# Kernel optimization log

Measured on AMD Instinct MI355X. Metric: run time of the kernel, lower is better.

The kernel has to match this reference:

```python
import math
import jax
import jax.numpy as jnp
import numpy as np

SEGMENT_SIZE = 2048   # w (init: segment_size)
DILATION_RATE = 4     # r (init: dilation_rate)
D_MODEL = 1024        # init: d_model


def _sparse_indices(n: int, w: int, r: int, head_idx: int) -> np.ndarray:
    """Static SparsifyIndices: per segment of size w, take tokens offset::r.
    Since r divides w, every segment yields exactly m=w//r indices (no -1 pad).
    Returns flat global token indices, shape (S*m,)."""
    S = n // w
    m = w // r
    off = head_idx % r
    seg_start = np.arange(S, dtype=np.int64)[:, None] * w      # (S,1)
    within = off + r * np.arange(m, dtype=np.int64)[None, :]   # (1,m)
    return (seg_start + within).reshape(-1)


def setup_inputs() -> dict:
    key = jax.random.key(0)
    x = jax.random.normal(key, (4, 8192, D_MODEL), dtype=jnp.float32)
    return {"x": x, "head_idx": 1}


def reference(x, head_idx):
    b, n0, d = x.shape
    w, r = SEGMENT_SIZE, DILATION_RATE
    pad = (-n0) % w
    if pad:
        x = jnp.pad(x, ((0, 0), (0, pad), (0, 0)))
    n = n0 + pad
    idx = _sparse_indices(n, w, r, int(head_idx))  # static, (S*m,)
    S, m = n // w, w // r

    # Gather dilated tokens per segment: (b, S, m, d)
    xg = x[:, idx, :].reshape(b, S, m, d)

    # Softmax attention within each sub-segment (q=k=v=xg)
    scores = jnp.einsum('bsid,bsjd->bsij', xg, xg) / math.sqrt(d)  # (b,S,m,m)
    probs = jax.nn.softmax(scores, axis=-1)
    att = jnp.einsum('bsij,bsjd->bsid', probs, xg).reshape(b, S * m, d)

    # MixOutputs: alpha-weighted scatter-add back to full sequence
    denoms = att.sum(-1)                                       # (b, S*m)
    denom_sums = jnp.zeros((b, n), x.dtype).at[:, idx].add(denoms)
    alphas = denoms / denom_sums[:, idx]                       # (b, S*m)
    out = jnp.zeros((b, n, d), x.dtype).at[:, idx, :].add(att * alphas[..., None])
    return out
```

## Files before the change

kernel.cpp:

```cpp
#include <hip/hip_runtime.h>
#include <hip/hip_bf16.h>


typedef __bf16 bf16_t;
typedef __bf16 bf16x8 __attribute__((ext_vector_type(8)));
typedef float floatx4 __attribute__((ext_vector_type(4)));

#define D_MODEL 1024
#define SEG_W   2048
#define RATE    4
#define M_SUB   512
#define NTOK    8192
#define NSEGT   16
#define XG_ELEMS ((long)NSEGT * M_SUB * D_MODEL)
#define S_ELEMS  ((long)NSEGT * M_SUB * M_SUB)

__device__ __forceinline__ void gload16(const bf16_t* g, bf16_t* l) {
    __builtin_amdgcn_global_load_lds(
        (const __attribute__((address_space(1))) void*)g,
        (__attribute__((address_space(3))) void*)l, 16, 0, 0);
}

__global__ __launch_bounds__(256) void zero_kernel(
    const int* __restrict__ hidp, float* __restrict__ out)
{
    const int off = ((hidp[0] % RATE) + RATE) % RATE;
    const int bid = blockIdx.x;
    const int b = bid / 6144, j = bid % 6144;
    const int q = j / 3, r2 = j % 3;
    const int t = 4 * q + r2 + (r2 >= off ? 1 : 0);
    float4 z = {0.f, 0.f, 0.f, 0.f};
    ((float4*)(out + ((long)b * NTOK + t) * D_MODEL))[threadIdx.x] = z;
}

__global__ __launch_bounds__(256) void gather_kernel(
    const float* __restrict__ x, const int* __restrict__ hidp,
    bf16_t* __restrict__ xg, bf16_t* __restrict__ xgT)
{
    const int off = ((hidp[0] % RATE) + RATE) % RATE;
    const int bid = blockIdx.x;
    const int seg = bid >> 7;
    const int rem = bid & 127;
    const int it  = rem >> 4;
    const int dt  = rem & 15;
    const int b   = seg >> 2, s = seg & 3;

    __shared__ ushort tile[64][65];

    const int t  = threadIdx.x;
    const int r  = t >> 2;
    const int cq = (t & 3) << 4;

    union U8 { bf16x8 v; ushort u[8]; };

    {
        const int  i   = it * 64 + r;
        const long tok = (long)s * SEG_W + off + 4L * i;
        const float* src = x + ((long)b * NTOK + tok) * D_MODEL + dt * 64 + cq;
        float4 f0 = ((const float4*)src)[0];
        float4 f1 = ((const float4*)src)[1];
        float4 f2 = ((const float4*)src)[2];
        float4 f3 = ((const float4*)src)[3];
        U8 lo, hi;
        lo.v[0]=(bf16_t)f0.x; lo.v[1]=(bf16_t)f0.y; lo.v[2]=(bf16_t)f0.z; lo.v[3]=(bf16_t)f0.w;
        lo.v[4]=(bf16_t)f1.x; lo.v[5]=(bf16_t)f1.y; lo.v[6]=(bf16_t)f1.z; lo.v[7]=(bf16_t)f1.w;
        hi.v[0]=(bf16_t)f2.x; hi.v[1]=(bf16_t)f2.y; hi.v[2]=(bf16_t)f2.z; hi.v[3]=(bf16_t)f2.w;
        hi.v[4]=(bf16_t)f3.x; hi.v[5]=(bf16_t)f3.y; hi.v[6]=(bf16_t)f3.z; hi.v[7]=(bf16_t)f3.w;
        bf16_t* dstg = xg + ((long)seg * M_SUB + i) * D_MODEL + dt * 64 + cq;
        *(bf16x8*)(dstg)     = lo.v;
        *(bf16x8*)(dstg + 8) = hi.v;
        #pragma unroll
        for (int j = 0; j < 8; ++j) { tile[r][cq + j] = lo.u[j]; tile[r][cq + 8 + j] = hi.u[j]; }
    }
    __syncthreads();
    {
        const int dc = r;
        const int iq = cq;
        U8 o0, o1;
        #pragma unroll
        for (int j = 0; j < 8; ++j) { o0.u[j] = tile[iq + j][dc]; o1.u[j] = tile[iq + 8 + j][dc]; }
        bf16_t* dstT = xgT + ((long)seg * D_MODEL + dt * 64 + dc) * M_SUB + it * 64 + iq;
        *(bf16x8*)(dstT)     = o0.v;
        *(bf16x8*)(dstT + 8) = o1.v;
    }
}

__global__ __launch_bounds__(256) void qk_kernel(
    const bf16_t* __restrict__ xg, bf16_t* __restrict__ S)
{
    const int bid = blockIdx.x;
    const int seg = bid >> 5;
    const int mt  = (bid >> 2) & 7;
    const int nt  = bid & 3;

    const int tid  = threadIdx.x;
    const int w    = tid >> 6;
    const int lane = tid & 63;
    const int l16  = lane & 15;
    const int quad = lane >> 4;
    const int wr   = w >> 1, wc = w & 1;

    __shared__ alignas(16) bf16_t As[64 * 32];
    __shared__ alignas(16) bf16_t Bs[128 * 32];

    const bf16_t* xseg = xg + (long)seg * M_SUB * D_MODEL;
    const bf16_t* ga  = xseg + (long)(mt * 64 + w * 16 + (lane >> 2)) * D_MODEL + (lane & 3) * 8;
    const bf16_t* gb0 = xseg + (long)(nt * 128 + (w * 2 + 0) * 16 + (lane >> 2)) * D_MODEL + (lane & 3) * 8;
    const bf16_t* gb1 = xseg + (long)(nt * 128 + (w * 2 + 1) * 16 + (lane >> 2)) * D_MODEL + (lane & 3) * 8;
    bf16_t* la  = &As[w * 512];
    bf16_t* lb0 = &Bs[(w * 2 + 0) * 512];
    bf16_t* lb1 = &Bs[(w * 2 + 1) * 512];

    floatx4 acc[2][4];
    #pragma unroll
    for (int i = 0; i < 2; ++i)
        #pragma unroll
        for (int j = 0; j < 4; ++j) acc[i][j] = (floatx4){0.f, 0.f, 0.f, 0.f};

    for (int kk = 0; kk < D_MODEL; kk += 32) {
        __syncthreads();
        gload16(ga  + kk, la);
        gload16(gb0 + kk, lb0);
        gload16(gb1 + kk, lb1);
        __syncthreads();

        bf16x8 Af[2], Bf[4];
        #pragma unroll
        for (int m2 = 0; m2 < 2; ++m2)
            Af[m2] = *(const bf16x8*)&As[(wr * 32 + m2 * 16 + l16) * 32 + quad * 8];
        #pragma unroll
        for (int n2 = 0; n2 < 4; ++n2)
            Bf[n2] = *(const bf16x8*)&Bs[(wc * 64 + n2 * 16 + l16) * 32 + quad * 8];
        #pragma unroll
        for (int m2 = 0; m2 < 2; ++m2)
            #pragma unroll
            for (int n2 = 0; n2 < 4; ++n2)
                acc[m2][n2] = __builtin_amdgcn_mfma_f32_16x16x32_bf16(Af[m2], Bf[n2], acc[m2][n2], 0, 0, 0);
    }

    const float scale = 0.03125f;
    bf16_t* Sseg = S + (long)seg * M_SUB * M_SUB;
    #pragma unroll
    for (int m2 = 0; m2 < 2; ++m2) {
        const int qrow = mt * 64 + wr * 32 + m2 * 16 + quad * 4;
        #pragma unroll
        for (int n2 = 0; n2 < 4; ++n2) {
            const int col = nt * 128 + wc * 64 + n2 * 16 + l16;
            #pragma unroll
            for (int rg = 0; rg < 4; ++rg)
                Sseg[(long)(qrow + rg) * M_SUB + col] = (bf16_t)(acc[m2][n2][rg] * scale);
        }
    }
}

__global__ __launch_bounds__(256) void softmax_kernel(bf16_t* __restrict__ S)
{
    const int row  = blockIdx.x * 4 + (threadIdx.x >> 6);
    const int lane = threadIdx.x & 63;
    bf16_t* p = S + (long)row * M_SUB + lane * 8;
    bf16x8 v = *(const bf16x8*)p;
    float f[8];
    #pragma unroll
    for (int j = 0; j < 8; ++j) f[j] = (float)v[j];
    float m = f[0];
    #pragma unroll
    for (int j = 1; j < 8; ++j) m = fmaxf(m, f[j]);
    #pragma unroll
    for (int d = 1; d < 64; d <<= 1) m = fmaxf(m, __shfl_xor(m, d, 64));
    float sum = 0.f;
    #pragma unroll
    for (int j = 0; j < 8; ++j) { f[j] = __expf(f[j] - m); sum += f[j]; }
    #pragma unroll
    for (int d = 1; d < 64; d <<= 1) sum += __shfl_xor(sum, d, 64);
    const float inv = 1.0f / sum;
    #pragma unroll
    for (int j = 0; j < 8; ++j) v[j] = (bf16_t)(f[j] * inv);
    *(bf16x8*)p = v;
}

__global__ __launch_bounds__(256) void pv_kernel(
    const bf16_t* __restrict__ S, const bf16_t* __restrict__ xgT,
    const int* __restrict__ hidp, float* __restrict__ out)
{
    const int off = ((hidp[0] % RATE) + RATE) % RATE;
    const int bid = blockIdx.x;
    const int seg = bid >> 5;
    const int mt  = (bid >> 3) & 3;
    const int nt  = bid & 7;
    const int b   = seg >> 2, s = seg & 3;

    const int tid  = threadIdx.x;
    const int w    = tid >> 6;
    const int lane = tid & 63;
    const int l16  = lane & 15;
    const int quad = lane >> 4;
    const int wr   = w >> 1, wc = w & 1;

    __shared__ alignas(16) bf16_t As[128 * 32];
    __shared__ alignas(16) bf16_t Bs[128 * 32];

    const bf16_t* Aseg = S   + (long)seg * M_SUB * M_SUB + (long)mt * 128 * M_SUB;
    const bf16_t* Bseg = xgT + (long)seg * D_MODEL * M_SUB + (long)nt * 128 * M_SUB;

    const bf16_t* ga0 = Aseg + (long)((w * 2 + 0) * 16 + (lane >> 2)) * M_SUB + (lane & 3) * 8;
    const bf16_t* ga1 = Aseg + (long)((w * 2 + 1) * 16 + (lane >> 2)) * M_SUB + (lane & 3) * 8;
    const bf16_t* gb0 = Bseg + (long)((w * 2 + 0) * 16 + (lane >> 2)) * M_SUB + (lane & 3) * 8;
    const bf16_t* gb1 = Bseg + (long)((w * 2 + 1) * 16 + (lane >> 2)) * M_SUB + (lane & 3) * 8;
    bf16_t* la0 = &As[(w * 2 + 0) * 512];
    bf16_t* la1 = &As[(w * 2 + 1) * 512];
    bf16_t* lb0 = &Bs[(w * 2 + 0) * 512];
    bf16_t* lb1 = &Bs[(w * 2 + 1) * 512];

    floatx4 acc[4][4];
    #pragma unroll
    for (int i = 0; i < 4; ++i)
        #pragma unroll
        for (int j = 0; j < 4; ++j) acc[i][j] = (floatx4){0.f, 0.f, 0.f, 0.f};

    for (int kk = 0; kk < M_SUB; kk += 32) {
        __syncthreads();
        gload16(ga0 + kk, la0);
        gload16(ga1 + kk, la1);
        gload16(gb0 + kk, lb0);
        gload16(gb1 + kk, lb1);
        __syncthreads();

        bf16x8 Af[4], Bf[4];
        #pragma unroll
        for (int m2 = 0; m2 < 4; ++m2)
            Af[m2] = *(const bf16x8*)&As[(wr * 64 + m2 * 16 + l16) * 32 + quad * 8];
        #pragma unroll
        for (int n2 = 0; n2 < 4; ++n2)
            Bf[n2] = *(const bf16x8*)&Bs[(wc * 64 + n2 * 16 + l16) * 32 + quad * 8];
        #pragma unroll
        for (int m2 = 0; m2 < 4; ++m2)
            #pragma unroll
            for (int n2 = 0; n2 < 4; ++n2)
                acc[m2][n2] = __builtin_amdgcn_mfma_f32_16x16x32_bf16(Af[m2], Bf[n2], acc[m2][n2], 0, 0, 0);
    }

    float* obase = out + (long)b * NTOK * D_MODEL;
    #pragma unroll
    for (int m2 = 0; m2 < 4; ++m2) {
        const int qrow0 = mt * 128 + wr * 64 + m2 * 16 + quad * 4;
        #pragma unroll
        for (int rg = 0; rg < 4; ++rg) {
            const long tok = (long)s * SEG_W + off + 4L * (qrow0 + rg);
            float* orow = obase + tok * D_MODEL;
            #pragma unroll
            for (int n2 = 0; n2 < 4; ++n2) {
                const int d = nt * 128 + wc * 64 + n2 * 16 + l16;
                orow[d] = acc[m2][n2][rg];
            }
        }
    }
}

extern "C" void kernel_launch(void* const* d_in, const int* in_sizes, int n_in,
                              void* d_out, int out_size, void* d_ws, size_t ws_size,
                              hipStream_t stream) {
    const float* x   = (const float*)d_in[0];
    const int*   hid = (const int*)d_in[1];
    float*       out = (float*)d_out;
    bf16_t* xg  = (bf16_t*)d_ws;
    bf16_t* xgT = xg + XG_ELEMS;
    bf16_t* S   = xgT + XG_ELEMS;

    zero_kernel<<<dim3(24576), dim3(256), 0, stream>>>(hid, out);
    gather_kernel<<<dim3(2048), dim3(256), 0, stream>>>(x, hid, xg, xgT);
    qk_kernel<<<dim3(512), dim3(256), 0, stream>>>(xg, S);
    softmax_kernel<<<dim3(2048), dim3(256), 0, stream>>>(S);
    pv_kernel<<<dim3(512), dim3(256), 0, stream>>>(S, xgT, hid, out);
}
```

Before: 254.5 us.

## Fuse zero-fill into PV kernel, widen K-tiles to 64 with XOR-swizzled LDS

Removes the separate zero kernel and writes the zeros for non-selected tokens from the PV kernel, each block covering its own 128-row by 128-column tile region, using nontemporal stores. Both GEMM kernels move from K-step 32 to K-step 64 with an XOR-swizzled LDS layout, halving the number of barrier pairs and avoiding bank conflicts on the fragment reads. Output stores also become nontemporal. The cost is more LDS per block, which may lower occupancy, and extra store traffic at the tail of the PV kernel.

```diff
diff --git a/kernel.cpp b/kernel.cpp
--- a/kernel.cpp
+++ b/kernel.cpp
@@ -13,24 +13,11 @@
 #define NTOK    8192
 #define NSEGT   16
 #define XG_ELEMS ((long)NSEGT * M_SUB * D_MODEL)
-#define S_ELEMS  ((long)NSEGT * M_SUB * M_SUB)
 
 __device__ __forceinline__ void gload16(const bf16_t* g, bf16_t* l) {
     __builtin_amdgcn_global_load_lds(
         (const __attribute__((address_space(1))) void*)g,
         (__attribute__((address_space(3))) void*)l, 16, 0, 0);
-}
-
-__global__ __launch_bounds__(256) void zero_kernel(
-    const int* __restrict__ hidp, float* __restrict__ out)
-{
-    const int off = ((hidp[0] % RATE) + RATE) % RATE;
-    const int bid = blockIdx.x;
-    const int b = bid / 6144, j = bid % 6144;
-    const int q = j / 3, r2 = j % 3;
-    const int t = 4 * q + r2 + (r2 >= off ? 1 : 0);
-    float4 z = {0.f, 0.f, 0.f, 0.f};
-    ((float4*)(out + ((long)b * NTOK + t) * D_MODEL))[threadIdx.x] = z;
 }
 
 __global__ __launch_bounds__(256) void gather_kernel(
@@ -99,17 +86,27 @@
     const int l16  = lane & 15;
     const int quad = lane >> 4;
     const int wr   = w >> 1, wc = w & 1;
-
-    __shared__ alignas(16) bf16_t As[64 * 32];
-    __shared__ alignas(16) bf16_t Bs[128 * 32];
+    const int rowin = lane >> 3;
+    const int cswz  = ((lane & 7) ^ rowin) * 8;
+    const int rsw   = l16 & 7;
+
+    __shared__ alignas(16) bf16_t As[64 * 64];
+    __shared__ alignas(16) bf16_t Bs[128 * 64];
 
     const bf16_t* xseg = xg + (long)seg * M_SUB * D_MODEL;
-    const bf16_t* ga  = xseg + (long)(mt * 64 + w * 16 + (lane >> 2)) * D_MODEL + (lane & 3) * 8;
-    const bf16_t* gb0 = xseg + (long)(nt * 128 + (w * 2 + 0) * 16 + (lane >> 2)) * D_MODEL + (lane & 3) * 8;
-    const bf16_t* gb1 = xseg + (long)(nt * 128 + (w * 2 + 1) * 16 + (lane >> 2)) * D_MODEL + (lane & 3) * 8;
-    bf16_t* la  = &As[w * 512];
-    bf16_t* lb0 = &Bs[(w * 2 + 0) * 512];
-    bf16_t* lb1 = &Bs[(w * 2 + 1) * 512];
+
+    const bf16_t* ga0 = xseg + (long)(mt * 64 + w * 16 + rowin) * D_MODEL + cswz;
+    const bf16_t* ga1 = ga0 + 8 * D_MODEL;
+    const bf16_t* gb0 = xseg + (long)(nt * 128 + w * 32 + rowin) * D_MODEL + cswz;
+    const bf16_t* gb1 = gb0 +  8 * D_MODEL;
+    const bf16_t* gb2 = gb0 + 16 * D_MODEL;
+    const bf16_t* gb3 = gb0 + 24 * D_MODEL;
+    bf16_t* la0 = &As[(w * 16 + 0) * 64];
+    bf16_t* la1 = &As[(w * 16 + 8) * 64];
+    bf16_t* lb0 = &Bs[(w * 32 + 0) * 64];
+    bf16_t* lb1 = &Bs[(w * 32 + 8) * 64];
+    bf16_t* lb2 = &Bs[(w * 32 + 16) * 64];
+    bf16_t* lb3 = &Bs[(w * 32 + 24) * 64];
 
     floatx4 acc[2][4];
     #pragma unroll
@@ -117,25 +114,32 @@
         #pragma unroll
         for (int j = 0; j < 4; ++j) acc[i][j] = (floatx4){0.f, 0.f, 0.f, 0.f};
 
-    for (int kk = 0; kk < D_MODEL; kk += 32) {
+    for (int kk = 0; kk < D_MODEL; kk += 64) {
         __syncthreads();
-        gload16(ga  + kk, la);
-        gload16(gb0 + kk, lb0);
-        gload16(gb1 + kk, lb1);
+        gload16(ga0 + kk, la0); gload16(ga1 + kk, la1);
+        gload16(gb0 + kk, lb0); gload16(gb1 + kk, lb1);
+        gload16(gb2 + kk, lb2); gload16(gb3 + kk, lb3);
         __syncthreads();
 
-        bf16x8 Af[2], Bf[4];
-        #pragma unroll
-        for (int m2 = 0; m2 < 2; ++m2)
-            Af[m2] = *(const bf16x8*)&As[(wr * 32 + m2 * 16 + l16) * 32 + quad * 8];
-        #pragma unroll
-        for (int n2 = 0; n2 < 4; ++n2)
-            Bf[n2] = *(const bf16x8*)&Bs[(wc * 64 + n2 * 16 + l16) * 32 + quad * 8];
-        #pragma unroll
-        for (int m2 = 0; m2 < 2; ++m2)
-            #pragma unroll
-            for (int n2 = 0; n2 < 4; ++n2)
-                acc[m2][n2] = __builtin_amdgcn_mfma_f32_16x16x32_bf16(Af[m2], Bf[n2], acc[m2][n2], 0, 0, 0);
+        #pragma unroll
+        for (int ks = 0; ks < 2; ++ks) {
+            bf16x8 Af[2], Bf[4];
+            #pragma unroll
+            for (int m2 = 0; m2 < 2; ++m2) {
+                const int row = wr * 32 + m2 * 16 + l16;
+                Af[m2] = *(const bf16x8*)&As[row * 64 + (((ks * 4 + quad) ^ rsw) * 8)];
+            }
+            #pragma unroll
+            for (int n2 = 0; n2 < 4; ++n2) {
+                const int row = wc * 64 + n2 * 16 + l16;
+                Bf[n2] = *(const bf16x8*)&Bs[row * 64 + (((ks * 4 + quad) ^ rsw) * 8)];
+            }
+            #pragma unroll
+            for (int m2 = 0; m2 < 2; ++m2)
+                #pragma unroll
+                for (int n2 = 0; n2 < 4; ++n2)
+                    acc[m2][n2] = __builtin_amdgcn_mfma_f32_16x16x32_bf16(Af[m2], Bf[n2], acc[m2][n2], 0, 0, 0);
+        }
     }
 
     const float scale = 0.03125f;
@@ -195,21 +199,32 @@
     const int l16  = lane & 15;
     const int quad = lane >> 4;
     const int wr   = w >> 1, wc = w & 1;
-
-    __shared__ alignas(16) bf16_t As[128 * 32];
-    __shared__ alignas(16) bf16_t Bs[128 * 32];
-
-    const bf16_t* Aseg = S   + (long)seg * M_SUB * M_SUB + (long)mt * 128 * M_SUB;
+    const int rowin = lane >> 3;
+    const int cswz  = ((lane & 7) ^ rowin) * 8;
+    const int rsw   = l16 & 7;
+
+    __shared__ alignas(16) bf16_t As[128 * 64];
+    __shared__ alignas(16) bf16_t Bs[128 * 64];
+
+    const bf16_t* Aseg = S   + (long)seg * M_SUB * M_SUB  + (long)mt * 128 * M_SUB;
     const bf16_t* Bseg = xgT + (long)seg * D_MODEL * M_SUB + (long)nt * 128 * M_SUB;
 
-    const bf16_t* ga0 = Aseg + (long)((w * 2 + 0) * 16 + (lane >> 2)) * M_SUB + (lane & 3) * 8;
-    const bf16_t* ga1 = Aseg + (long)((w * 2 + 1) * 16 + (lane >> 2)) * M_SUB + (lane & 3) * 8;
-    const bf16_t* gb0 = Bseg + (long)((w * 2 + 0) * 16 + (lane >> 2)) * M_SUB + (lane & 3) * 8;
-    const bf16_t* gb1 = Bseg + (long)((w * 2 + 1) * 16 + (lane >> 2)) * M_SUB + (lane & 3) * 8;
-    bf16_t* la0 = &As[(w * 2 + 0) * 512];
-    bf16_t* la1 = &As[(w * 2 + 1) * 512];
-    bf16_t* lb0 = &Bs[(w * 2 + 0) * 512];
-    bf16_t* lb1 = &Bs[(w * 2 + 1) * 512];
+    const bf16_t* ga0 = Aseg + (long)(w * 32 + rowin) * M_SUB + cswz;
+    const bf16_t* ga1 = ga0 +  8 * M_SUB;
+    const bf16_t* ga2 = ga0 + 16 * M_SUB;
+    const bf16_t* ga3 = ga0 + 24 * M_SUB;
+    const bf16_t* gb0 = Bseg + (long)(w * 32 + rowin) * M_SUB + cswz;
+    const bf16_t* gb1 = gb0 +  8 * M_SUB;
+    const bf16_t* gb2 = gb0 + 16 * M_SUB;
+    const bf16_t* gb3 = gb0 + 24 * M_SUB;
+    bf16_t* la0 = &As[(w * 32 + 0) * 64];
+    bf16_t* la1 = &As[(w * 32 + 8) * 64];
+    bf16_t* la2 = &As[(w * 32 + 16) * 64];
+    bf16_t* la3 = &As[(w * 32 + 24) * 64];
+    bf16_t* lb0 = &Bs[(w * 32 + 0) * 64];
+    bf16_t* lb1 = &Bs[(w * 32 + 8) * 64];
+    bf16_t* lb2 = &Bs[(w * 32 + 16) * 64];
+    bf16_t* lb3 = &Bs[(w * 32 + 24) * 64];
 
     floatx4 acc[4][4];
     #pragma unroll
@@ -217,26 +232,33 @@
         #pragma unroll
         for (int j = 0; j < 4; ++j) acc[i][j] = (floatx4){0.f, 0.f, 0.f, 0.f};
 
-    for (int kk = 0; kk < M_SUB; kk += 32) {
+    for (int kk = 0; kk < M_SUB; kk += 64) {
         __syncthreads();
-        gload16(ga0 + kk, la0);
-        gload16(ga1 + kk, la1);
-        gload16(gb0 + kk, lb0);
-        gload16(gb1 + kk, lb1);
+        gload16(ga0 + kk, la0); gload16(ga1 + kk, la1);
+        gload16(ga2 + kk, la2); gload16(ga3 + kk, la3);
+        gload16(gb0 + kk, lb0); gload16(gb1 + kk, lb1);
+        gload16(gb2 + kk, lb2); gload16(gb3 + kk, lb3);
         __syncthreads();
 
-        bf16x8 Af[4], Bf[4];
-        #pragma unroll
-        for (int m2 = 0; m2 < 4; ++m2)
-            Af[m2] = *(const bf16x8*)&As[(wr * 64 + m2 * 16 + l16) * 32 + quad * 8];
-        #pragma unroll
-        for (int n2 = 0; n2 < 4; ++n2)
-            Bf[n2] = *(const bf16x8*)&Bs[(wc * 64 + n2 * 16 + l16) * 32 + quad * 8];
-        #pragma unroll
-        for (int m2 = 0; m2 < 4; ++m2)
-            #pragma unroll
-            for (int n2 = 0; n2 < 4; ++n2)
-                acc[m2][n2] = __builtin_amdgcn_mfma_f32_16x16x32_bf16(Af[m2], Bf[n2], acc[m2][n2], 0, 0, 0);
+        #pragma unroll
+        for (int ks = 0; ks < 2; ++ks) {
+            bf16x8 Af[4], Bf[4];
+            #pragma unroll
+            for (int m2 = 0; m2 < 4; ++m2) {
+                const int row = wr * 64 + m2 * 16 + l16;
+                Af[m2] = *(const bf16x8*)&As[row * 64 + (((ks * 4 + quad) ^ rsw) * 8)];
+            }
+            #pragma unroll
+            for (int n2 = 0; n2 < 4; ++n2) {
+                const int row = wc * 64 + n2 * 16 + l16;
+                Bf[n2] = *(const bf16x8*)&Bs[row * 64 + (((ks * 4 + quad) ^ rsw) * 8)];
+            }
+            #pragma unroll
+            for (int m2 = 0; m2 < 4; ++m2)
+                #pragma unroll
+                for (int n2 = 0; n2 < 4; ++n2)
+                    acc[m2][n2] = __builtin_amdgcn_mfma_f32_16x16x32_bf16(Af[m2], Bf[n2], acc[m2][n2], 0, 0, 0);
+        }
     }
 
     float* obase = out + (long)b * NTOK * D_MODEL;
@@ -250,8 +272,23 @@
             #pragma unroll
             for (int n2 = 0; n2 < 4; ++n2) {
                 const int d = nt * 128 + wc * 64 + n2 * 16 + l16;
-                orow[d] = acc[m2][n2][rg];
-            }
+                __builtin_nontemporal_store(acc[m2][n2][rg], &orow[d]);
+            }
+        }
+    }
+
+    {
+        const floatx4 z = {0.f, 0.f, 0.f, 0.f};
+        const int zr = tid >> 5;
+        const int zc = tid & 31;
+        #pragma unroll 4
+        for (int p = 0; p < 48; ++p) {
+            const int j = p * 8 + zr;
+            const int q = j / 3, e = j % 3;
+            const int delta = e + (e >= off ? 1 : 0);
+            const long tok = (long)s * SEG_W + 4L * (mt * 128 + q) + delta;
+            float* dst = obase + tok * D_MODEL + nt * 128 + zc * 4;
+            __builtin_nontemporal_store(z, (floatx4*)dst);
         }
     }
 }
@@ -266,7 +303,6 @@
     bf16_t* xgT = xg + XG_ELEMS;
     bf16_t* S   = xgT + XG_ELEMS;
 
-    zero_kernel<<<dim3(24576), dim3(256), 0, stream>>>(hid, out);
     gather_kernel<<<dim3(2048), dim3(256), 0, stream>>>(x, hid, xg, xgT);
     qk_kernel<<<dim3(512), dim3(256), 0, stream>>>(xg, S);
     softmax_kernel<<<dim3(2048), dim3(256), 0, stream>>>(S);
```

Result: faster. 248.5 us (-2.4%).
